# Optimization experiments

Hardware: AMD Instinct MI355X
Metric: run time of the kernel (lower is better)

The kernel has to match this reference:

```python
import jax, jax.numpy as jnp
import numpy as np

EPS = 1e-3  # Keras BatchNormalization default epsilon
PARTITIONS = 4


def setup_inputs() -> dict:
    key = jax.random.key(0)
    k1, k2 = jax.random.split(key)
    B, H, W, C = 256, 32, 32, 256
    x = jax.random.normal(k1, (B, H, W, C), dtype=jnp.float32)
    gamma = jnp.ones((PARTITIONS, C), dtype=jnp.float32)
    beta = jnp.zeros((PARTITIONS, C), dtype=jnp.float32)
    perm = jax.random.permutation(k2, B).astype(jnp.int32)
    return {"x": x, "gamma": gamma, "beta": beta, "perm": perm}


def reference(x, gamma, beta, perm):
    B, H, W, C = x.shape
    P = PARTITIONS
    ps = B // P  # partition size (B divisible by P)
    # shuffle gather along batch
    shuffled = x[perm]                               # [B,H,W,C]
    parts = shuffled.reshape(P, ps, H, W, C)         # [P,ps,H,W,C]
    # per-partition, per-channel batch statistics (training-mode BN, biased var)
    mean = jnp.mean(parts, axis=(1, 2, 3), keepdims=True)  # [P,1,1,1,C]
    var = jnp.var(parts, axis=(1, 2, 3), keepdims=True)    # [P,1,1,1,C]
    g = gamma[:, None, None, None, :]
    b = beta[:, None, None, None, :]
    normalized = (parts - mean) * jax.lax.rsqrt(var + EPS) * g + b
    shuffled_normalized = normalized.reshape(B, H, W, C)
    # inverse gather (un-shuffle)
    inv_perm = jnp.argsort(perm)
    return shuffled_normalized[inv_perm]
```

## Files before the change

kernel.cpp:

```cpp
#include <hip/hip_runtime.h>

#define EPS 0.001f
#define HW_POS 1024
#define NCH 256
#define NCG 64
#define NB 256
#define NP 4
#define PS 64
#define SPLIT 4
#define POS_PER_BLOCK (HW_POS / SPLIT)
#define N_PER_PC 65536.0f

__global__ __launch_bounds__(256) void k_zero(float* __restrict__ acc) {
    const int i = threadIdx.x;
    #pragma unroll
    for (int k = 0; k < 8; ++k) acc[k * 256 + i] = 0.f;
}

__global__ __launch_bounds__(256) void k_partial(const float4* __restrict__ x,
                                                 const int* __restrict__ perm,
                                                 float* __restrict__ asum,
                                                 float* __restrict__ asq) {
    const int slot  = blockIdx.x;
    const int j     = slot >> 2;
    const int chunk = slot & (SPLIT - 1);
    const int b     = perm[j];
    const int p     = j >> 6;
    const int t     = threadIdx.x;
    const int cg    = t & 63;
    const int srow  = t >> 6;

    const float4* xb = x + (size_t)b * (HW_POS * NCG);
    const int s0 = chunk * POS_PER_BLOCK;

    float4 s = make_float4(0.f, 0.f, 0.f, 0.f);
    float4 q = make_float4(0.f, 0.f, 0.f, 0.f);
    #pragma unroll 8
    for (int si = s0 + srow; si < s0 + POS_PER_BLOCK; si += 4) {
        float4 v = xb[(size_t)si * NCG + cg];
        s.x += v.x; s.y += v.y; s.z += v.z; s.w += v.w;
        q.x += v.x * v.x; q.y += v.y * v.y; q.z += v.z * v.z; q.w += v.w * v.w;
    }

    __shared__ float4 ls[4][64];
    __shared__ float4 lq[4][64];
    ls[srow][cg] = s;
    lq[srow][cg] = q;
    __syncthreads();

    if (srow == 0) {
        float4 a0 = ls[0][cg], a1 = ls[1][cg], a2 = ls[2][cg], a3 = ls[3][cg];
        float4 b0 = lq[0][cg], b1 = lq[1][cg], b2 = lq[2][cg], b3 = lq[3][cg];
        float ts[4] = { a0.x + a1.x + a2.x + a3.x,
                        a0.y + a1.y + a2.y + a3.y,
                        a0.z + a1.z + a2.z + a3.z,
                        a0.w + a1.w + a2.w + a3.w };
        float tq[4] = { b0.x + b1.x + b2.x + b3.x,
                        b0.y + b1.y + b2.y + b3.y,
                        b0.z + b1.z + b2.z + b3.z,
                        b0.w + b1.w + b2.w + b3.w };
        float* sp = asum + p * NCH + cg * 4;
        float* qp = asq  + p * NCH + cg * 4;
        #pragma unroll
        for (int k = 0; k < 4; ++k) {
            atomicAdd(sp + k, ts[k]);
            atomicAdd(qp + k, tq[k]);
        }
    }
}

__global__ __launch_bounds__(256) void k_norm(const float4* __restrict__ x,
                                              const float* __restrict__ asum,
                                              const float* __restrict__ asq,
                                              const float* __restrict__ gamma,
                                              const float* __restrict__ beta,
                                              const int* __restrict__ perm,
                                              float4* __restrict__ out) {
    const int blk   = (int)gridDim.x - 1 - (int)blockIdx.x;
    const int j     = blk >> 2;
    const int chunk = blk & (SPLIT - 1);
    const int b     = perm[j];
    const int p     = j >> 6;
    const int t     = threadIdx.x;
    const int cg    = t & 63;
    const int srow  = t >> 6;

    float4 sc, sh;
    {
        float scv[4], shv[4];
        #pragma unroll
        for (int k = 0; k < 4; ++k) {
            const int c   = cg * 4 + k;
            const float s = asum[p * NCH + c];
            const float q = asq [p * NCH + c];
            const float mean = s * (1.0f / N_PER_PC);
            const float var  = q * (1.0f / N_PER_PC) - mean * mean;
            const float inv  = rsqrtf(var + EPS);
            const float g    = gamma[p * NCH + c];
            scv[k] = g * inv;
            shv[k] = beta[p * NCH + c] - mean * scv[k];
        }
        sc = make_float4(scv[0], scv[1], scv[2], scv[3]);
        sh = make_float4(shv[0], shv[1], shv[2], shv[3]);
    }

    const float4* xb = x   + (size_t)b * (HW_POS * NCG);
    float4*       ob = out + (size_t)b * (HW_POS * NCG);
    const int s0 = chunk * POS_PER_BLOCK;

    #pragma unroll 8
    for (int si = s0 + srow; si < s0 + POS_PER_BLOCK; si += 4) {
        float4 v = xb[(size_t)si * NCG + cg];
        v.x = v.x * sc.x + sh.x;
        v.y = v.y * sc.y + sh.y;
        v.z = v.z * sc.z + sh.z;
        v.w = v.w * sc.w + sh.w;
        ob[(size_t)si * NCG + cg] = v;
    }
}

extern "C" void kernel_launch(void* const* d_in, const int* in_sizes, int n_in,
                              void* d_out, int out_size, void* d_ws, size_t ws_size,
                              hipStream_t stream) {
    const float* x     = (const float*)d_in[0];
    const float* gamma = (const float*)d_in[1];
    const float* beta  = (const float*)d_in[2];
    const int*   perm  = (const int*)d_in[3];
    float* out = (float*)d_out;

    float* asum = (float*)d_ws;
    float* asq  = asum + NP * NCH;

    k_zero<<<1, 256, 0, stream>>>(asum);
    k_partial<<<NB * SPLIT, 256, 0, stream>>>((const float4*)x, perm, asum, asq);
    k_norm<<<NB * SPLIT, 256, 0, stream>>>((const float4*)x, asum, asq,
                                           gamma, beta, perm, (float4*)out);
}
```

Baseline: 506.3 us.

## Fuse zero, stats, and normalize into one cooperative kernel with grid sync

Replaces the three separate launches (zero accumulators, partial stats, normalize) with a single cooperative kernel that uses grid-wide syncs between phases. In the normalize phase each block walks its own slice in reverse so recently read data may still be in cache, and it uses nontemporal loads and stores. This removes launch gaps and lets the second read of x hit the cache, at the cost of grid sync overhead and a requirement that all 1024 blocks be co-resident at 4 blocks per CU.

```diff
diff --git a/kernel.cpp b/kernel.cpp
--- a/kernel.cpp
+++ b/kernel.cpp
@@ -1,4 +1,7 @@
 #include <hip/hip_runtime.h>
+#include <hip/hip_cooperative_groups.h>
+
+namespace cg = cooperative_groups;
 
 #define EPS 0.001f
 #define HW_POS 1024
@@ -6,29 +9,37 @@
 #define NCG 64
 #define NB 256
 #define NP 4
-#define PS 64
 #define SPLIT 4
 #define POS_PER_BLOCK (HW_POS / SPLIT)
 #define N_PER_PC 65536.0f
+#define NBLK (NB * SPLIT)
 
-__global__ __launch_bounds__(256) void k_zero(float* __restrict__ acc) {
-    const int i = threadIdx.x;
-    #pragma unroll
-    for (int k = 0; k < 8; ++k) acc[k * 256 + i] = 0.f;
-}
+typedef float f32x4 __attribute__((ext_vector_type(4)));
 
-__global__ __launch_bounds__(256) void k_partial(const float4* __restrict__ x,
-                                                 const int* __restrict__ perm,
-                                                 float* __restrict__ asum,
-                                                 float* __restrict__ asq) {
-    const int slot  = blockIdx.x;
-    const int j     = slot >> 2;
-    const int chunk = slot & (SPLIT - 1);
+__global__ __launch_bounds__(256, 4)
+void k_fused(const float4* __restrict__ x,
+             const float*  __restrict__ gamma,
+             const float*  __restrict__ beta,
+             const int*    __restrict__ perm,
+             float4*       __restrict__ out,
+             float*        __restrict__ asum,
+             float*        __restrict__ asq) {
+    cg::grid_group grid = cg::this_grid();
+
+    const int blk   = (int)blockIdx.x;
+    const int j     = blk >> 2;
+    const int chunk = blk & (SPLIT - 1);
     const int b     = perm[j];
     const int p     = j >> 6;
-    const int t     = threadIdx.x;
-    const int cg    = t & 63;
+    const int t     = (int)threadIdx.x;
+    const int cgp   = t & 63;
     const int srow  = t >> 6;
+
+    if (blk == 0) {
+        #pragma unroll
+        for (int k = 0; k < 8; ++k) asum[k * 256 + t] = 0.f;
+    }
+    grid.sync();
 
     const float4* xb = x + (size_t)b * (HW_POS * NCG);
     const int s0 = chunk * POS_PER_BLOCK;
@@ -37,20 +48,20 @@
     float4 q = make_float4(0.f, 0.f, 0.f, 0.f);
     #pragma unroll 8
     for (int si = s0 + srow; si < s0 + POS_PER_BLOCK; si += 4) {
-        float4 v = xb[(size_t)si * NCG + cg];
+        float4 v = xb[(size_t)si * NCG + cgp];
         s.x += v.x; s.y += v.y; s.z += v.z; s.w += v.w;
         q.x += v.x * v.x; q.y += v.y * v.y; q.z += v.z * v.z; q.w += v.w * v.w;
     }
 
     __shared__ float4 ls[4][64];
     __shared__ float4 lq[4][64];
-    ls[srow][cg] = s;
-    lq[srow][cg] = q;
+    ls[srow][cgp] = s;
+    lq[srow][cgp] = q;
     __syncthreads();
 
     if (srow == 0) {
-        float4 a0 = ls[0][cg], a1 = ls[1][cg], a2 = ls[2][cg], a3 = ls[3][cg];
-        float4 b0 = lq[0][cg], b1 = lq[1][cg], b2 = lq[2][cg], b3 = lq[3][cg];
+        float4 a0 = ls[0][cgp], a1 = ls[1][cgp], a2 = ls[2][cgp], a3 = ls[3][cgp];
+        float4 b0 = lq[0][cgp], b1 = lq[1][cgp], b2 = lq[2][cgp], b3 = lq[3][cgp];
         float ts[4] = { a0.x + a1.x + a2.x + a3.x,
                         a0.y + a1.y + a2.y + a3.y,
                         a0.z + a1.z + a2.z + a3.z,
@@ -59,42 +70,28 @@
                         b0.y + b1.y + b2.y + b3.y,
                         b0.z + b1.z + b2.z + b3.z,
                         b0.w + b1.w + b2.w + b3.w };
-        float* sp = asum + p * NCH + cg * 4;
-        float* qp = asq  + p * NCH + cg * 4;
+        float* sp = asum + p * NCH + cgp * 4;
+        float* qp = asq  + p * NCH + cgp * 4;
         #pragma unroll
         for (int k = 0; k < 4; ++k) {
             atomicAdd(sp + k, ts[k]);
             atomicAdd(qp + k, tq[k]);
         }
     }
-}
 
-__global__ __launch_bounds__(256) void k_norm(const float4* __restrict__ x,
-                                              const float* __restrict__ asum,
-                                              const float* __restrict__ asq,
-                                              const float* __restrict__ gamma,
-                                              const float* __restrict__ beta,
-                                              const int* __restrict__ perm,
-                                              float4* __restrict__ out) {
-    const int blk   = (int)gridDim.x - 1 - (int)blockIdx.x;
-    const int j     = blk >> 2;
-    const int chunk = blk & (SPLIT - 1);
-    const int b     = perm[j];
-    const int p     = j >> 6;
-    const int t     = threadIdx.x;
-    const int cg    = t & 63;
-    const int srow  = t >> 6;
+    __threadfence();
+    grid.sync();
 
     float4 sc, sh;
     {
         float scv[4], shv[4];
         #pragma unroll
         for (int k = 0; k < 4; ++k) {
-            const int c   = cg * 4 + k;
-            const float s = asum[p * NCH + c];
-            const float q = asq [p * NCH + c];
-            const float mean = s * (1.0f / N_PER_PC);
-            const float var  = q * (1.0f / N_PER_PC) - mean * mean;
+            const int c    = cgp * 4 + k;
+            const float sv = asum[p * NCH + c];
+            const float qv = asq [p * NCH + c];
+            const float mean = sv * (1.0f / N_PER_PC);
+            const float var  = qv * (1.0f / N_PER_PC) - mean * mean;
             const float inv  = rsqrtf(var + EPS);
             const float g    = gamma[p * NCH + c];
             scv[k] = g * inv;
@@ -104,35 +101,34 @@
         sh = make_float4(shv[0], shv[1], shv[2], shv[3]);
     }
 
-    const float4* xb = x   + (size_t)b * (HW_POS * NCG);
-    float4*       ob = out + (size_t)b * (HW_POS * NCG);
-    const int s0 = chunk * POS_PER_BLOCK;
-
+    float4* ob = out + (size_t)b * (HW_POS * NCG);
     #pragma unroll 8
-    for (int si = s0 + srow; si < s0 + POS_PER_BLOCK; si += 4) {
-        float4 v = xb[(size_t)si * NCG + cg];
-        v.x = v.x * sc.x + sh.x;
-        v.y = v.y * sc.y + sh.y;
-        v.z = v.z * sc.z + sh.z;
-        v.w = v.w * sc.w + sh.w;
-        ob[(size_t)si * NCG + cg] = v;
+    for (int si = s0 + POS_PER_BLOCK - 4 + srow; si >= s0; si -= 4) {
+        const size_t idx = (size_t)si * NCG + cgp;
+        f32x4 v = __builtin_nontemporal_load((const f32x4*)(xb + idx));
+        f32x4 r;
+        r.x = v.x * sc.x + sh.x;
+        r.y = v.y * sc.y + sh.y;
+        r.z = v.z * sc.z + sh.z;
+        r.w = v.w * sc.w + sh.w;
+        __builtin_nontemporal_store(r, (f32x4*)(ob + idx));
     }
 }
 
 extern "C" void kernel_launch(void* const* d_in, const int* in_sizes, int n_in,
                               void* d_out, int out_size, void* d_ws, size_t ws_size,
                               hipStream_t stream) {
-    const float* x     = (const float*)d_in[0];
-    const float* gamma = (const float*)d_in[1];
-    const float* beta  = (const float*)d_in[2];
-    const int*   perm  = (const int*)d_in[3];
-    float* out = (float*)d_out;
+    const float4* x     = (const float4*)d_in[0];
+    const float*  gamma = (const float*)d_in[1];
+    const float*  beta  = (const float*)d_in[2];
+    const int*    perm  = (const int*)d_in[3];
+    float4* out = (float4*)d_out;
 
     float* asum = (float*)d_ws;
     float* asq  = asum + NP * NCH;
 
-    k_zero<<<1, 256, 0, stream>>>(asum);
-    k_partial<<<NB * SPLIT, 256, 0, stream>>>((const float4*)x, perm, asum, asq);
-    k_norm<<<NB * SPLIT, 256, 0, stream>>>((const float4*)x, asum, asq,
-                                           gamma, beta, perm, (float4*)out);
+    void* args[] = { (void*)&x, (void*)&gamma, (void*)&beta, (void*)&perm,
+                     (void*)&out, (void*)&asum, (void*)&asq };
+    hipLaunchCooperativeKernel((void*)k_fused, dim3(NBLK), dim3(256),
+                               args, 0, stream);
 }
```

New measurement: 785.7 us. +55.2%, slower.
